# Optimization experiments

Hardware: AMD Instinct MI355X
Metric: run time of the kernel (lower is better)

The kernel has to match this reference:

```python
import jax, jax.numpy as jnp
import numpy as np

BN_EPS = 1e-5


def setup_inputs() -> dict:
    key = jax.random.key(0)
    ks = jax.random.split(key, 5)
    b, c, seq, K = 16, 128, 16384, 64
    x = jax.random.normal(ks[0], (b, c, 1, seq), dtype=jnp.float32)
    std = 1.0 / np.sqrt(K * c)
    codewords = jax.random.uniform(ks[1], (K, c), dtype=jnp.float32, minval=-std, maxval=std)
    smoothing = jax.random.uniform(ks[2], (K,), dtype=jnp.float32, minval=-1.0, maxval=0.0)
    bn_weight = jnp.ones((K,), dtype=jnp.float32)
    bn_bias = jnp.zeros((K,), dtype=jnp.float32)
    fc_w = jax.random.normal(ks[3], (c, c), dtype=jnp.float32) * (1.0 / np.sqrt(c))
    fc_b = jax.random.uniform(ks[4], (c,), dtype=jnp.float32, minval=-1.0 / np.sqrt(c), maxval=1.0 / np.sqrt(c))
    return {"x": x, "codewords": codewords, "smoothing": smoothing,
            "bn_weight": bn_weight, "bn_bias": bn_bias, "fc_w": fc_w, "fc_b": fc_b}


def reference(x, codewords, smoothing, bn_weight, bn_bias, fc_w, fc_b):
    # x: (b, c, 1, seq); codewords: (K, c); smoothing: (K,)
    xs = jnp.transpose(x[:, :, 0, :], (0, 2, 1))          # (b, seq, c)
    # squared distances ||x - cw||^2 via expansion (avoids (b,seq,K,c) tensor)
    x2 = jnp.sum(xs * xs, axis=-1)                         # (b, seq)
    cw2 = jnp.sum(codewords * codewords, axis=-1)          # (K,)
    cross = jnp.einsum('bsc,kc->bsk', xs, codewords)       # (b, seq, K)
    d2 = x2[:, :, None] - 2.0 * cross + cw2[None, None, :]
    a = jax.nn.softmax(smoothing[None, None, :] * d2, axis=2)  # (b, seq, K)
    # e = sum_s a * (x - cw)  (residual aggregation, expansion-free)
    e = jnp.einsum('bsk,bsc->bkc', a, xs) - jnp.sum(a, axis=1)[:, :, None] * codewords[None]  # (b, K, c)
    # BatchNorm1d over K features (training-mode batch stats over dims (b, c))
    mean = jnp.mean(e, axis=(0, 2), keepdims=True)
    var = jnp.var(e, axis=(0, 2), keepdims=True)
    e_bn = (e - mean) / jnp.sqrt(var + BN_EPS) * bn_weight[None, :, None] + bn_bias[None, :, None]
    e_norm = jnp.mean(jax.nn.relu(e_bn), axis=1)           # (b, c)
    scale = jax.nn.sigmoid(e_norm @ fc_w.T + fc_b)         # (b, c)
    return x * scale[:, :, None, None]
```

## Files before the change

kernel.cpp:

```cpp
#include <hip/hip_runtime.h>

typedef unsigned int u32;
typedef unsigned short u16;
typedef unsigned long long u64;

typedef float f32x4 __attribute__((ext_vector_type(4)));
typedef short bf16x8 __attribute__((ext_vector_type(8)));

#define B_   16
#define C_   128
#define SEQ_ 16384
#define K_   64
#define TS_  64
#define NT_  8
#define CHUNK_ 512

constexpr int OFF_EACC = 0;
constexpr int OFF_ASUM = 131072;
constexpr int OFF_SM   = 136192;
constexpr int OFF_SMC2 = 136256;
constexpr int OFF_SCALE= 136320;

__device__ __forceinline__ u16 f2bf(float f) {
    u32 b = __float_as_uint(f);
    return (u16)((b + 0x7FFFu + ((b >> 16) & 1u)) >> 16);
}
__device__ __forceinline__ float scrub(float v) {
    return fminf(fmaxf(v, -1.0e4f), 1.0e4f);
}

__global__ void k0_prep(const float* __restrict__ cw, const float* __restrict__ sm,
                        float* __restrict__ ws) {
    const int t = threadIdx.x;
    if (t < K_) {
        float s2 = 0.f;
        for (int c = 0; c < C_; ++c) { float f = cw[t * C_ + c]; s2 += f * f; }
        float smv = sm[t];
        ws[OFF_SM + t] = smv;
        ws[OFF_SMC2 + t] = smv * s2;
    }
}

__global__ __launch_bounds__(256, 2)
void k1_encode(const float* __restrict__ xg, const float* __restrict__ cwg, float* ws) {
    __shared__ __align__(16) u16 xsc_h[TS_ * C_];
    __shared__ __align__(16) u16 xsc_l[TS_ * C_];
    __shared__ __align__(16) u16 xcs[C_ * 72];
    __shared__ __align__(16) u16 alds[K_ * 72];
    __shared__ __align__(16) float x2part[16 * 68];
    __shared__ float x2s[TS_];

    const int t    = threadIdx.x;
    const int lane = t & 63;
    const int w    = t >> 6;
    const int lk   = lane & 15;
    const int lg   = lane >> 4;
    const int b      = blockIdx.x >> 5;
    const int s_base = (blockIdx.x & 31) * CHUNK_;

    bf16x8 cwf[4][4];
#pragma unroll
    for (int nt = 0; nt < 4; ++nt)
#pragma unroll
      for (int ks = 0; ks < 4; ++ks) {
        const float* p = cwg + (size_t)(lk + 16*nt) * C_ + 8*lg + 32*ks;
        float4 v0 = *(const float4*)p;
        float4 v1 = *(const float4*)(p + 4);
        bf16x8 f;
        f[0]=(short)f2bf(v0.x); f[1]=(short)f2bf(v0.y); f[2]=(short)f2bf(v0.z); f[3]=(short)f2bf(v0.w);
        f[4]=(short)f2bf(v1.x); f[5]=(short)f2bf(v1.y); f[6]=(short)f2bf(v1.z); f[7]=(short)f2bf(v1.w);
        cwf[nt][ks] = f;
      }
    float smk[4], smc2k[4];
#pragma unroll
    for (int nt = 0; nt < 4; ++nt) {
        smk[nt]   = ws[OFF_SM   + lk + 16*nt];
        smc2k[nt] = ws[OFF_SMC2 + lk + 16*nt];
    }

    f32x4 acc2[4][2] = {};
    float asacc[4] = {0.f,0.f,0.f,0.f};

    const int sm_ = t & 15;
    const int sg_ = t >> 4;

    float4 vc[8];
    {
        const float* xb = xg + (size_t)(b * C_ + 8*sm_) * SEQ_ + s_base + 4*sg_;
#pragma unroll
        for (int r = 0; r < 8; ++r) vc[r] = *(const float4*)(xb + (size_t)r * SEQ_);
    }

    for (int tile = 0; tile < NT_; ++tile) {
        const int st = s_base + tile * TS_;
        __syncthreads();

        {
            u16 H[8][4], L[8][4];
            float x2p[4] = {0.f,0.f,0.f,0.f};
#pragma unroll
            for (int r = 0; r < 8; ++r) {
                float fa[4] = {vc[r].x, vc[r].y, vc[r].z, vc[r].w};
#pragma unroll
                for (int i = 0; i < 4; ++i) {
                    float f = fa[i];
                    u32 bu = __float_as_uint(f);
                    u16 hh = (u16)(bu >> 16);
                    float fh = __uint_as_float((u32)hh << 16);
                    u16 ll = (u16)(__float_as_uint(f - fh) >> 16);
                    H[r][i] = hh; L[r][i] = ll;
                    x2p[i] = fmaf(f, f, x2p[i]);
                }
            }
            if (tile + 1 < NT_) {
                const float* xb = xg + (size_t)(b * C_ + 8*sm_) * SEQ_ + (st + TS_) + 4*sg_;
#pragma unroll
                for (int r = 0; r < 8; ++r) vc[r] = *(const float4*)(xb + (size_t)r * SEQ_);
            }
#pragma unroll
            for (int r = 0; r < 8; ++r) {
                int c = 8*sm_ + r;
                u64 pk = (u64)H[r][0] | ((u64)H[r][1] << 16) | ((u64)H[r][2] << 32) | ((u64)H[r][3] << 48);
                *(u64*)&xcs[c * 72 + ((4*sg_) ^ ((sm_ & 7) << 3))] = pk;
            }
#pragma unroll
            for (int i = 0; i < 4; ++i) {
                int s = 4*sg_ + i;
                u32 idx = (u32)(s * C_ + 8*sm_) ^ ((u32)(s & 15) << 3);
                uint4 hw, lw;
                hw.x = (u32)H[0][i] | ((u32)H[1][i] << 16);
                hw.y = (u32)H[2][i] | ((u32)H[3][i] << 16);
                hw.z = (u32)H[4][i] | ((u32)H[5][i] << 16);
                hw.w = (u32)H[6][i] | ((u32)H[7][i] << 16);
                lw.x = (u32)L[0][i] | ((u32)L[1][i] << 16);
                lw.y = (u32)L[2][i] | ((u32)L[3][i] << 16);
                lw.z = (u32)L[4][i] | ((u32)L[5][i] << 16);
                lw.w = (u32)L[6][i] | ((u32)L[7][i] << 16);
                *(uint4*)&xsc_h[idx] = hw;
                *(uint4*)&xsc_l[idx] = lw;
            }
            *(float4*)&x2part[sm_ * 68 + 4*sg_] = make_float4(x2p[0], x2p[1], x2p[2], x2p[3]);
        }
        __syncthreads();

        if (t < TS_) {
            float s2 = 0.f;
#pragma unroll
            for (int p = 0; p < 16; ++p) s2 += x2part[p * 68 + t];
            x2s[t] = s2;
        }

        f32x4 d1[4];
        {
            const int sA = 16*w + lk;
            bf16x8 ah[4], al[4];
#pragma unroll
            for (int ks = 0; ks < 4; ++ks) {
                u32 idx = (u32)(sA * C_ + 8*lg + 32*ks) ^ ((u32)(sA & 15) << 3);
                ah[ks] = *(const bf16x8*)&xsc_h[idx];
                al[ks] = *(const bf16x8*)&xsc_l[idx];
            }
#pragma unroll
            for (int nt = 0; nt < 4; ++nt) {
                f32x4 a = {0.f, 0.f, 0.f, 0.f};
#pragma unroll
                for (int ks = 0; ks < 4; ++ks) {
                    a = __builtin_amdgcn_mfma_f32_16x16x32_bf16(ah[ks], cwf[nt][ks], a, 0, 0, 0);
                    a = __builtin_amdgcn_mfma_f32_16x16x32_bf16(al[ks], cwf[nt][ks], a, 0, 0, 0);
                }
                d1[nt] = a;
            }
        }
        __syncthreads();

        {
            float x2r[4], mx[4], pp[4][4], inv[4];
#pragma unroll
            for (int r = 0; r < 4; ++r) { x2r[r] = x2s[16*w + 4*lg + r]; mx[r] = -1.0e30f; }
#pragma unroll
            for (int nt = 0; nt < 4; ++nt)
#pragma unroll
              for (int r = 0; r < 4; ++r) {
                float lv = fmaf(smk[nt], x2r[r] - 2.0f * d1[nt][r], smc2k[nt]);
                lv = scrub(lv);
                pp[nt][r] = lv;
                mx[r] = fmaxf(mx[r], lv);
              }
#pragma unroll
            for (int r = 0; r < 4; ++r) {
                mx[r] = fmaxf(mx[r], __shfl_xor(mx[r], 1));
                mx[r] = fmaxf(mx[r], __shfl_xor(mx[r], 2));
                mx[r] = fmaxf(mx[r], __shfl_xor(mx[r], 4));
                mx[r] = fmaxf(mx[r], __shfl_xor(mx[r], 8));
            }
            float sum[4] = {0.f,0.f,0.f,0.f};
#pragma unroll
            for (int nt = 0; nt < 4; ++nt)
#pragma unroll
              for (int r = 0; r < 4; ++r) {
                float e = __expf(pp[nt][r] - mx[r]);
                pp[nt][r] = e;
                sum[r] += e;
              }
#pragma unroll
            for (int r = 0; r < 4; ++r) {
                sum[r] += __shfl_xor(sum[r], 1);
                sum[r] += __shfl_xor(sum[r], 2);
                sum[r] += __shfl_xor(sum[r], 4);
                sum[r] += __shfl_xor(sum[r], 8);
                inv[r] = 1.0f / sum[r];
            }
#pragma unroll
            for (int nt = 0; nt < 4; ++nt) {
                u16 q[4];
                float sloc = 0.f;
#pragma unroll
                for (int r = 0; r < 4; ++r) {
                    float a = pp[nt][r] * inv[r];
                    sloc += a;
                    q[r] = f2bf(a);
                }
                asacc[nt] += sloc;
                u64 pk = (u64)q[0] | ((u64)q[1] << 16) | ((u64)q[2] << 32) | ((u64)q[3] << 48);
                *(u64*)&alds[(lk + 16*nt) * 72 + 16*w + 4*lg] = pk;
            }
        }
        __syncthreads();

#pragma unroll
        for (int ss = 0; ss < 2; ++ss) {
            bf16x8 aA[4], bX[2];
#pragma unroll
            for (int mt = 0; mt < 4; ++mt)
                aA[mt] = *(const bf16x8*)&alds[(lk + 16*mt) * 72 + 8*lg + 32*ss];
#pragma unroll
            for (int n = 0; n < 2; ++n) {
                int c = lk + 16*(2*w + n);
                u32 idx = (u32)(c * 72) + (((u32)(8*lg + 32*ss)) ^ (((u32)(c >> 3) & 7) << 3));
                bX[n] = *(const bf16x8*)&xcs[idx];
            }
#pragma unroll
            for (int mt = 0; mt < 4; ++mt)
#pragma unroll
              for (int n = 0; n < 2; ++n)
                acc2[mt][n] = __builtin_amdgcn_mfma_f32_16x16x32_bf16(aA[mt], bX[n], acc2[mt][n], 0, 0, 0);
        }
    }

    float* eacc = ws + OFF_EACC;
#pragma unroll
    for (int mt = 0; mt < 4; ++mt)
#pragma unroll
      for (int n = 0; n < 2; ++n) {
        const int c = lk + 16*(2*w + n);
#pragma unroll
        for (int r = 0; r < 4; ++r) {
            int k = 16*mt + 4*lg + r;
            atomicAdd(&eacc[(b * K_ + k) * C_ + c], acc2[mt][n][r]);
        }
      }
#pragma unroll
    for (int nt = 0; nt < 4; ++nt) {
        float v = asacc[nt];
        v += __shfl_xor(v, 16);
        v += __shfl_xor(v, 32);
        if (lane < 16) atomicAdd(&ws[OFF_ASUM + b * K_ + lk + 16*nt], v);
    }
}

__global__ __launch_bounds__(1024)
void k2_bn_fc(const float* __restrict__ cw,
              const float* __restrict__ bnw, const float* __restrict__ bnb,
              const float* __restrict__ fcw, const float* __restrict__ fcb,
              float* ws) {
    __shared__ float fcw_s[C_][C_ + 1];
    __shared__ float enorm_s[B_ * C_];
    __shared__ float redA[K_][16], redB[K_][16];
    __shared__ float scale_k[K_], bias_k[K_];
    const int t = threadIdx.x;
    const float* eacc = ws + OFF_EACC;
    const float* asum = ws + OFF_ASUM;
    for (int i = 0; i < 16; ++i) {
        int idx = i * 1024 + t;
        fcw_s[idx >> 7][idx & 127] = fcw[idx];
    }
    {
        int k = t >> 4, part = t & 15;
        float sv = 0.f, sq2 = 0.f;
        for (int i = 0; i < 128; ++i) {
            int flat = part + (i << 4);
            int bb = flat >> 7, c = flat & 127;
            float e = eacc[(bb * K_ + k) * C_ + c] - asum[bb * K_ + k] * cw[k * C_ + c];
            sv += e; sq2 += e * e;
        }
        redA[k][part] = sv; redB[k][part] = sq2;
    }
    __syncthreads();
    if (t < K_) {
        float sv = 0.f, sq2 = 0.f;
        for (int p = 0; p < 16; ++p) { sv += redA[t][p]; sq2 += redB[t][p]; }
        float mean = sv * (1.f / 2048.f);
        float var  = sq2 * (1.f / 2048.f) - mean * mean;
        float rstd = rsqrtf(fmaxf(var, 0.f) + 1e-5f);
        float g = bnw[t] * rstd;
        scale_k[t] = g;
        bias_k[t]  = bnb[t] - mean * g;
    }
    __syncthreads();
    for (int r = 0; r < 2; ++r) {
        int u = r * 1024 + t;
        int bb = u >> 7, c = u & 127;
        float s = 0.f;
        for (int k = 0; k < K_; ++k) {
            float e = eacc[(bb * K_ + k) * C_ + c] - asum[bb * K_ + k] * cw[k * C_ + c];
            float bnv = e * scale_k[k] + bias_k[k];
            bnv = fminf(fmaxf(bnv, 0.f), 1.0e6f);
            s += bnv;
        }
        enorm_s[u] = s * (1.f / 64.f);
    }
    __syncthreads();
    for (int r = 0; r < 2; ++r) {
        int u = r * 1024 + t;
        int bb = u >> 7, c = u & 127;
        float accv = fcb[c];
        for (int cc = 0; cc < C_; ++cc)
            accv += enorm_s[(bb << 7) + cc] * fcw_s[c][cc];
        ws[OFF_SCALE + u] = 1.f / (1.f + __expf(-accv));
    }
}

__global__ __launch_bounds__(256)
void k3_scale(const float4* __restrict__ xg, float4* __restrict__ outg,
              const float* __restrict__ ws) {
    const int bc = blockIdx.x;
    const float sc = ws[OFF_SCALE + bc];
    const float4* xr = xg + (size_t)bc * (SEQ_ / 4);
    float4* orow = outg + (size_t)bc * (SEQ_ / 4);
    const int t = threadIdx.x;
    for (int i = 0; i < SEQ_ / 4 / 256; ++i) {
        float4 v = xr[i * 256 + t];
        v.x *= sc; v.y *= sc; v.z *= sc; v.w *= sc;
        orow[i * 256 + t] = v;
    }
}

extern "C" void kernel_launch(void* const* d_in, const int* in_sizes, int n_in,
                              void* d_out, int out_size, void* d_ws, size_t ws_size,
                              hipStream_t stream) {
    const float* x   = (const float*)d_in[0];
    const float* cw  = (const float*)d_in[1];
    const float* sm  = (const float*)d_in[2];
    const float* bnw = (const float*)d_in[3];
    const float* bnb = (const float*)d_in[4];
    const float* fcw = (const float*)d_in[5];
    const float* fcb = (const float*)d_in[6];
    float* ws = (float*)d_ws;

    hipMemsetAsync(ws, 0, (size_t)(OFF_ASUM + B_ * K_) * sizeof(float), stream);
    k0_prep<<<1, 256, 0, stream>>>(cw, sm, ws);
    k1_encode<<<B_ * (SEQ_ / CHUNK_), 256, 0, stream>>>(x, cw, ws);
    k2_bn_fc<<<1, 1024, 0, stream>>>(cw, bnw, bnb, fcw, fcb, ws);
    k3_scale<<<B_ * C_, 256, 0, stream>>>((const float4*)x, (float4*)d_out, ws);
}
```

Baseline: 347.1 us.

## Restructure encode pipeline and split BN/FC reduction into parallel kernels

The encode kernel drops the transposed x tile and the x2 partial buffers in shared memory. x² row sums are now reduced with wave shuffles, and the second GEMM reads x directly from global memory into bf16 fragments, deferred by one tile so it overlaps the next tile's distance GEMM. Two barriers per tile are removed and occupancy is raised to 3 blocks per CU. The single-block BN/FC kernel is split into a per-K statistics kernel and a per-batch FC kernel, which spreads that serial tail work across many CUs. In exchange, x is re-read from global memory in the second GEMM, and the x² shuffle reduce depends on how the 16-lane groups line up with the MFMA row layout.

After: 386.9 us. 11.5% more time.

```diff
diff --git a/kernel.cpp b/kernel.cpp
--- a/kernel.cpp
+++ b/kernel.cpp
@@ -17,6 +17,8 @@
 
 constexpr int OFF_EACC = 0;
 constexpr int OFF_ASUM = 131072;
+constexpr int OFF_BNS  = 132096;
+constexpr int OFF_BNB  = 132160;
 constexpr int OFF_SM   = 136192;
 constexpr int OFF_SMC2 = 136256;
 constexpr int OFF_SCALE= 136320;
@@ -41,14 +43,11 @@
     }
 }
 
-__global__ __launch_bounds__(256, 2)
+__global__ __launch_bounds__(256, 3)
 void k1_encode(const float* __restrict__ xg, const float* __restrict__ cwg, float* ws) {
     __shared__ __align__(16) u16 xsc_h[TS_ * C_];
     __shared__ __align__(16) u16 xsc_l[TS_ * C_];
-    __shared__ __align__(16) u16 xcs[C_ * 72];
-    __shared__ __align__(16) u16 alds[K_ * 72];
-    __shared__ __align__(16) float x2part[16 * 68];
-    __shared__ float x2s[TS_];
+    __shared__ __align__(16) u16 alds[K_ * TS_];
 
     const int t    = threadIdx.x;
     const int lane = t & 63;
@@ -84,12 +83,38 @@
     const int sm_ = t & 15;
     const int sg_ = t >> 4;
 
+    auto gemm2 = [&](int stp) {
+#pragma unroll
+        for (int ss = 0; ss < 2; ++ss) {
+            bf16x8 aA[4];
+#pragma unroll
+            for (int mt = 0; mt < 4; ++mt)
+                aA[mt] = *(const bf16x8*)&alds[(lk + 16*mt) * TS_ + ((8*lg + 32*ss) ^ ((lk & 7) << 3))];
+#pragma unroll
+            for (int n = 0; n < 2; ++n) {
+                const float* xr = xg + (size_t)(b * C_ + lk + 16*(2*w + n)) * SEQ_ + stp + 8*lg + 32*ss;
+                float4 v0 = *(const float4*)xr;
+                float4 v1 = *(const float4*)(xr + 4);
+                bf16x8 bx;
+                ((u32*)&bx)[0] = (__float_as_uint(v0.x) >> 16) | (__float_as_uint(v0.y) & 0xFFFF0000u);
+                ((u32*)&bx)[1] = (__float_as_uint(v0.z) >> 16) | (__float_as_uint(v0.w) & 0xFFFF0000u);
+                ((u32*)&bx)[2] = (__float_as_uint(v1.x) >> 16) | (__float_as_uint(v1.y) & 0xFFFF0000u);
+                ((u32*)&bx)[3] = (__float_as_uint(v1.z) >> 16) | (__float_as_uint(v1.w) & 0xFFFF0000u);
+#pragma unroll
+                for (int mt = 0; mt < 4; ++mt)
+                    acc2[mt][n] = __builtin_amdgcn_mfma_f32_16x16x32_bf16(aA[mt], bx, acc2[mt][n], 0, 0, 0);
+            }
+        }
+    };
+
     float4 vc[8];
     {
         const float* xb = xg + (size_t)(b * C_ + 8*sm_) * SEQ_ + s_base + 4*sg_;
 #pragma unroll
         for (int r = 0; r < 8; ++r) vc[r] = *(const float4*)(xb + (size_t)r * SEQ_);
     }
+
+    float x2red[4];
 
     for (int tile = 0; tile < NT_; ++tile) {
         const int st = s_base + tile * TS_;
@@ -118,10 +143,13 @@
                 for (int r = 0; r < 8; ++r) vc[r] = *(const float4*)(xb + (size_t)r * SEQ_);
             }
 #pragma unroll
-            for (int r = 0; r < 8; ++r) {
-                int c = 8*sm_ + r;
-                u64 pk = (u64)H[r][0] | ((u64)H[r][1] << 16) | ((u64)H[r][2] << 32) | ((u64)H[r][3] << 48);
-                *(u64*)&xcs[c * 72 + ((4*sg_) ^ ((sm_ & 7) << 3))] = pk;
+            for (int i = 0; i < 4; ++i) {
+                float v = x2p[i];
+                v += __shfl_xor(v, 1);
+                v += __shfl_xor(v, 2);
+                v += __shfl_xor(v, 4);
+                v += __shfl_xor(v, 8);
+                x2red[i] = v;
             }
 #pragma unroll
             for (int i = 0; i < 4; ++i) {
@@ -139,49 +167,35 @@
                 *(uint4*)&xsc_h[idx] = hw;
                 *(uint4*)&xsc_l[idx] = lw;
             }
-            *(float4*)&x2part[sm_ * 68 + 4*sg_] = make_float4(x2p[0], x2p[1], x2p[2], x2p[3]);
-        }
+        }
+        if (tile > 0) gemm2(st - TS_);
         __syncthreads();
 
-        if (t < TS_) {
-            float s2 = 0.f;
-#pragma unroll
-            for (int p = 0; p < 16; ++p) s2 += x2part[p * 68 + t];
-            x2s[t] = s2;
-        }
-
-        f32x4 d1[4];
+        f32x4 d1[4] = {};
         {
             const int sA = 16*w + lk;
-            bf16x8 ah[4], al[4];
 #pragma unroll
             for (int ks = 0; ks < 4; ++ks) {
                 u32 idx = (u32)(sA * C_ + 8*lg + 32*ks) ^ ((u32)(sA & 15) << 3);
-                ah[ks] = *(const bf16x8*)&xsc_h[idx];
-                al[ks] = *(const bf16x8*)&xsc_l[idx];
-            }
-#pragma unroll
-            for (int nt = 0; nt < 4; ++nt) {
-                f32x4 a = {0.f, 0.f, 0.f, 0.f};
-#pragma unroll
-                for (int ks = 0; ks < 4; ++ks) {
-                    a = __builtin_amdgcn_mfma_f32_16x16x32_bf16(ah[ks], cwf[nt][ks], a, 0, 0, 0);
-                    a = __builtin_amdgcn_mfma_f32_16x16x32_bf16(al[ks], cwf[nt][ks], a, 0, 0, 0);
+                bf16x8 ah = *(const bf16x8*)&xsc_h[idx];
+                bf16x8 al = *(const bf16x8*)&xsc_l[idx];
+#pragma unroll
+                for (int nt = 0; nt < 4; ++nt) {
+                    d1[nt] = __builtin_amdgcn_mfma_f32_16x16x32_bf16(ah, cwf[nt][ks], d1[nt], 0, 0, 0);
+                    d1[nt] = __builtin_amdgcn_mfma_f32_16x16x32_bf16(al, cwf[nt][ks], d1[nt], 0, 0, 0);
                 }
-                d1[nt] = a;
-            }
-        }
-        __syncthreads();
+            }
+        }
 
         {
-            float x2r[4], mx[4], pp[4][4], inv[4];
-#pragma unroll
-            for (int r = 0; r < 4; ++r) { x2r[r] = x2s[16*w + 4*lg + r]; mx[r] = -1.0e30f; }
+            float mx[4], pp[4][4], inv[4];
+#pragma unroll
+            for (int r = 0; r < 4; ++r) mx[r] = -1.0e30f;
 #pragma unroll
             for (int nt = 0; nt < 4; ++nt)
 #pragma unroll
               for (int r = 0; r < 4; ++r) {
-                float lv = fmaf(smk[nt], x2r[r] - 2.0f * d1[nt][r], smc2k[nt]);
+                float lv = fmaf(smk[nt], x2red[r] - 2.0f * d1[nt][r], smc2k[nt]);
                 lv = scrub(lv);
                 pp[nt][r] = lv;
                 mx[r] = fmaxf(mx[r], lv);
@@ -222,30 +236,12 @@
                 }
                 asacc[nt] += sloc;
                 u64 pk = (u64)q[0] | ((u64)q[1] << 16) | ((u64)q[2] << 32) | ((u64)q[3] << 48);
-                *(u64*)&alds[(lk + 16*nt) * 72 + 16*w + 4*lg] = pk;
-            }
-        }
-        __syncthreads();
-
-#pragma unroll
-        for (int ss = 0; ss < 2; ++ss) {
-            bf16x8 aA[4], bX[2];
-#pragma unroll
-            for (int mt = 0; mt < 4; ++mt)
-                aA[mt] = *(const bf16x8*)&alds[(lk + 16*mt) * 72 + 8*lg + 32*ss];
-#pragma unroll
-            for (int n = 0; n < 2; ++n) {
-                int c = lk + 16*(2*w + n);
-                u32 idx = (u32)(c * 72) + (((u32)(8*lg + 32*ss)) ^ (((u32)(c >> 3) & 7) << 3));
-                bX[n] = *(const bf16x8*)&xcs[idx];
-            }
-#pragma unroll
-            for (int mt = 0; mt < 4; ++mt)
-#pragma unroll
-              for (int n = 0; n < 2; ++n)
-                acc2[mt][n] = __builtin_amdgcn_mfma_f32_16x16x32_bf16(aA[mt], bX[n], acc2[mt][n], 0, 0, 0);
-        }
-    }
+                *(u64*)&alds[(lk + 16*nt) * TS_ + (((u32)(16*w + 4*lg)) ^ ((u32)(lk & 7) << 3))] = pk;
+            }
+        }
+    }
+    __syncthreads();
+    gemm2(s_base + (NT_ - 1) * TS_);
 
     float* eacc = ws + OFF_EACC;
 #pragma unroll
@@ -268,65 +264,82 @@
     }
 }
 
-__global__ __launch_bounds__(1024)
-void k2_bn_fc(const float* __restrict__ cw,
-              const float* __restrict__ bnw, const float* __restrict__ bnb,
-              const float* __restrict__ fcw, const float* __restrict__ fcb,
-              float* ws) {
-    __shared__ float fcw_s[C_][C_ + 1];
-    __shared__ float enorm_s[B_ * C_];
-    __shared__ float redA[K_][16], redB[K_][16];
-    __shared__ float scale_k[K_], bias_k[K_];
+__global__ __launch_bounds__(256)
+void k2a_stats(const float* __restrict__ cw,
+               const float* __restrict__ bnw, const float* __restrict__ bnb,
+               float* ws) {
+    const int k = blockIdx.x;
     const int t = threadIdx.x;
+    const int lane = t & 63, w = t >> 6;
+    __shared__ float redS[4], redQ[4];
     const float* eacc = ws + OFF_EACC;
     const float* asum = ws + OFF_ASUM;
-    for (int i = 0; i < 16; ++i) {
-        int idx = i * 1024 + t;
-        fcw_s[idx >> 7][idx & 127] = fcw[idx];
-    }
-    {
-        int k = t >> 4, part = t & 15;
-        float sv = 0.f, sq2 = 0.f;
-        for (int i = 0; i < 128; ++i) {
-            int flat = part + (i << 4);
-            int bb = flat >> 7, c = flat & 127;
-            float e = eacc[(bb * K_ + k) * C_ + c] - asum[bb * K_ + k] * cw[k * C_ + c];
-            sv += e; sq2 += e * e;
-        }
-        redA[k][part] = sv; redB[k][part] = sq2;
-    }
-    __syncthreads();
-    if (t < K_) {
-        float sv = 0.f, sq2 = 0.f;
-        for (int p = 0; p < 16; ++p) { sv += redA[t][p]; sq2 += redB[t][p]; }
-        float mean = sv * (1.f / 2048.f);
-        float var  = sq2 * (1.f / 2048.f) - mean * mean;
+    float sv = 0.f, sq = 0.f;
+#pragma unroll
+    for (int u = t; u < 512; u += 256) {
+        int bb = u >> 5, c4 = u & 31;
+        float a = asum[bb * K_ + k];
+        float4 ev = *(const float4*)&eacc[(bb * K_ + k) * C_ + 4*c4];
+        float4 cv = *(const float4*)&cw[k * C_ + 4*c4];
+        float e0 = ev.x - a * cv.x, e1 = ev.y - a * cv.y;
+        float e2 = ev.z - a * cv.z, e3 = ev.w - a * cv.w;
+        sv += e0 + e1 + e2 + e3;
+        sq += e0*e0 + e1*e1 + e2*e2 + e3*e3;
+    }
+#pragma unroll
+    for (int m = 1; m < 64; m <<= 1) {
+        sv += __shfl_xor(sv, m);
+        sq += __shfl_xor(sq, m);
+    }
+    if (lane == 0) { redS[w] = sv; redQ[w] = sq; }
+    __syncthreads();
+    if (t == 0) {
+        float s = redS[0]+redS[1]+redS[2]+redS[3];
+        float q = redQ[0]+redQ[1]+redQ[2]+redQ[3];
+        float mean = s * (1.f / 2048.f);
+        float var  = q * (1.f / 2048.f) - mean * mean;
         float rstd = rsqrtf(fmaxf(var, 0.f) + 1e-5f);
-        float g = bnw[t] * rstd;
-        scale_k[t] = g;
-        bias_k[t]  = bnb[t] - mean * g;
-    }
-    __syncthreads();
-    for (int r = 0; r < 2; ++r) {
-        int u = r * 1024 + t;
-        int bb = u >> 7, c = u & 127;
-        float s = 0.f;
-        for (int k = 0; k < K_; ++k) {
-            float e = eacc[(bb * K_ + k) * C_ + c] - asum[bb * K_ + k] * cw[k * C_ + c];
-            float bnv = e * scale_k[k] + bias_k[k];
-            bnv = fminf(fmaxf(bnv, 0.f), 1.0e6f);
-            s += bnv;
-        }
-        enorm_s[u] = s * (1.f / 64.f);
-    }
-    __syncthreads();
-    for (int r = 0; r < 2; ++r) {
-        int u = r * 1024 + t;
-        int bb = u >> 7, c = u & 127;
-        float accv = fcb[c];
-        for (int cc = 0; cc < C_; ++cc)
-            accv += enorm_s[(bb << 7) + cc] * fcw_s[c][cc];
-        ws[OFF_SCALE + u] = 1.f / (1.f + __expf(-accv));
+        float g = bnw[k] * rstd;
+        ws[OFF_BNS + k] = g;
+        ws[OFF_BNB + k] = bnb[k] - mean * g;
+    }
+}
+
+__global__ __launch_bounds__(256)
+void k2b_fc(const float* __restrict__ cw,
+            const float* __restrict__ fcw, const float* __restrict__ fcb,
+            float* ws) {
+    __shared__ float enorm_s[C_];
+    __shared__ float red2[C_];
+    const int b = blockIdx.x;
+    const int t = threadIdx.x;
+    const int c = t & 127, h = t >> 7;
+    const float* eacc = ws + OFF_EACC;
+    float s = 0.f;
+    for (int kk = 0; kk < 32; ++kk) {
+        int k = 32*h + kk;
+        float e = eacc[(b * K_ + k) * C_ + c] - ws[OFF_ASUM + b * K_ + k] * cw[k * C_ + c];
+        float bnv = e * ws[OFF_BNS + k] + ws[OFF_BNB + k];
+        s += fminf(fmaxf(bnv, 0.f), 1.0e6f);
+    }
+    if (h) red2[c] = s;
+    __syncthreads();
+    if (!h) enorm_s[c] = (s + red2[c]) * (1.f / 64.f);
+    __syncthreads();
+    float acc = 0.f;
+    const float4* fw = (const float4*)&fcw[c * C_ + 64*h];
+#pragma unroll
+    for (int q = 0; q < 16; ++q) {
+        float4 wv = fw[q];
+        int ci = 64*h + 4*q;
+        acc += enorm_s[ci] * wv.x + enorm_s[ci+1] * wv.y + enorm_s[ci+2] * wv.z + enorm_s[ci+3] * wv.w;
+    }
+    __syncthreads();
+    if (h) red2[c] = acc;
+    __syncthreads();
+    if (!h) {
+        float o = fcb[c] + acc + red2[c];
+        ws[OFF_SCALE + b * C_ + c] = 1.f / (1.f + __expf(-o));
     }
 }
 
@@ -360,6 +373,7 @@
     hipMemsetAsync(ws, 0, (size_t)(OFF_ASUM + B_ * K_) * sizeof(float), stream);
     k0_prep<<<1, 256, 0, stream>>>(cw, sm, ws);
     k1_encode<<<B_ * (SEQ_ / CHUNK_), 256, 0, stream>>>(x, cw, ws);
-    k2_bn_fc<<<1, 1024, 0, stream>>>(cw, bnw, bnb, fcw, fcb, ws);
+    k2a_stats<<<K_, 256, 0, stream>>>(cw, bnw, bnb, ws);
+    k2b_fc<<<B_, 256, 0, stream>>>(cw, fcw, fcb, ws);
     k3_scale<<<B_ * C_, 256, 0, stream>>>((const float4*)x, (float4*)d_out, ws);
 }
```
